# Performance work log

Measured on AMD Instinct MI355X. Metric: run time of the kernel, lower is better.

## Reference

```python
import jax, jax.numpy as jnp
import numpy as np

D = 512  # feature_dim


def setup_inputs() -> dict:
    key = jax.random.key(0)
    ks = jax.random.split(key, 16)
    B, S, P, NP = 64, 4096, 4, 4
    s = 1.0 / np.sqrt(D)
    inp = {
        "trajectory_features": jax.random.normal(ks[0], (B, S, D), dtype=jnp.float32),
        "primitive_sequence": jax.random.randint(ks[1], (P,), 0, NP),
        # primitive embedding table (num_primitives, D)
        "emb": jax.random.normal(ks[2], (NP, D), dtype=jnp.float32),
        # q/k/v projections, stored as (in, out) so y = x @ W + b
        "Wq": jax.random.uniform(ks[3], (D, D), minval=-s, maxval=s, dtype=jnp.float32),
        "bq": jax.random.uniform(ks[4], (D,), minval=-s, maxval=s, dtype=jnp.float32),
        "Wk": jax.random.uniform(ks[5], (D, D), minval=-s, maxval=s, dtype=jnp.float32),
        "bk": jax.random.uniform(ks[6], (D,), minval=-s, maxval=s, dtype=jnp.float32),
        "Wv": jax.random.uniform(ks[7], (D, D), minval=-s, maxval=s, dtype=jnp.float32),
        "bv": jax.random.uniform(ks[8], (D,), minval=-s, maxval=s, dtype=jnp.float32),
        # credit estimator MLP: Linear(2D,64) -> ReLU -> Linear(64,1) -> Sigmoid
        "W1": jax.random.uniform(ks[9], (2 * D, 64), minval=-1 / np.sqrt(2 * D), maxval=1 / np.sqrt(2 * D), dtype=jnp.float32),
        "b1": jax.random.uniform(ks[10], (64,), minval=-1 / np.sqrt(2 * D), maxval=1 / np.sqrt(2 * D), dtype=jnp.float32),
        "W2": jax.random.uniform(ks[11], (64, 1), minval=-0.125, maxval=0.125, dtype=jnp.float32),
        "b2": jax.random.uniform(ks[12], (1,), minval=-0.125, maxval=0.125, dtype=jnp.float32),
    }
    return inp


def reference(trajectory_features, primitive_sequence, emb, Wq, bq, Wk, bk, Wv, bv, W1, b1, W2, b2):
    # primitive embeddings: (P, D)
    prim = emb[primitive_sequence]
    # projections
    q = trajectory_features @ Wq + bq          # (B, S, D)
    k = prim @ Wk + bk                         # (P, D) -- shared across batch
    v = prim @ Wv + bv                         # (P, D)
    # tiny-K cross attention
    scores = jnp.einsum("bsd,pd->bsp", q, k) / jnp.sqrt(jnp.float32(D))
    attn = jax.nn.softmax(scores, axis=-1)     # (B, S, P)
    weighted = jnp.einsum("bsp,pd->bsd", attn, v)
    # concat + MLP credit head
    combined = jnp.concatenate([trajectory_features, weighted], axis=-1)  # (B, S, 2D)
    h = jax.nn.relu(combined @ W1 + b1)
    credit = jax.nn.sigmoid(h @ W2 + b2)[..., 0]  # (B, S)
    return credit, attn
```

## Files before the change

kernel.cpp:

```cpp
#include <hip/hip_runtime.h>
#include <hip/hip_bf16.h>

#define DD 512
#define OFF_K   0
#define OFF_V   8192
#define OFF_C   16384
#define OFF_VB  16448
#define OFF_KQ  17472
#define OFF_W1F 25664

typedef __attribute__((ext_vector_type(8))) __bf16 bf16x8;
typedef __attribute__((ext_vector_type(8))) float f32x8;
typedef __attribute__((ext_vector_type(4))) float f32x4;
typedef unsigned short u16;

__device__ __forceinline__ u16 f2bf(float f) {
  unsigned u = __builtin_bit_cast(unsigned, f);
  u += 0x7fffu + ((u >> 16) & 1u);
  return (u16)(u >> 16);
}

__global__ void prep_kv(const float* __restrict__ emb, const int* __restrict__ seq,
                        const float* __restrict__ Wk, const float* __restrict__ bk,
                        const float* __restrict__ Wv, const float* __restrict__ bv,
                        float* __restrict__ ws_kv) {
  __shared__ float red[8][64];
  const int b = blockIdx.x;
  const int kind = b >> 5, p = (b >> 3) & 3, dc = b & 7;
  const int dl = threadIdx.x & 63, jg = threadIdx.x >> 6;
  const int d = dc * 64 + dl;
  const float* W = kind ? Wv : Wk;
  const float* bias = kind ? bv : bk;
  const float* pr = emb + seq[p] * DD + jg * 64;
  const float* Wp = W + (size_t)(jg * 64) * DD + d;
  float a0 = 0.f, a1 = 0.f, a2 = 0.f, a3 = 0.f;
  #pragma unroll 4
  for (int j = 0; j < 64; j += 4) {
    a0 += pr[j]     * Wp[(size_t)j * DD];
    a1 += pr[j + 1] * Wp[(size_t)(j + 1) * DD];
    a2 += pr[j + 2] * Wp[(size_t)(j + 2) * DD];
    a3 += pr[j + 3] * Wp[(size_t)(j + 3) * DD];
  }
  red[jg][dl] = (a0 + a1) + (a2 + a3);
  __syncthreads();
  if (jg == 0) {
    float s = red[0][dl];
    #pragma unroll
    for (int g = 1; g < 8; ++g) s += red[g][dl];
    ws_kv[kind * 2048 + p * 512 + d] = s + bias[d];
  }
}

__global__ void prep_frag(const float* __restrict__ Wq, const float* __restrict__ bq,
                          const float* __restrict__ W1, char* __restrict__ ws) {
  const float* kk = (const float*)(ws + OFF_K);
  const float* vv = (const float*)(ws + OFF_V);
  const int b = blockIdx.x;
  const int lane = threadIdx.x & 63;
  const int wv = threadIdx.x >> 6;

  if (b < 128) {
    const int dg = b * 4 + wv;
    const f32x8 wqv = *(const f32x8*)(Wq + (size_t)dg * DD + lane * 8);
    float a[4];
    #pragma unroll
    for (int p = 0; p < 4; ++p) {
      const f32x8 kv = *(const f32x8*)(kk + p * 512 + lane * 8);
      float s = 0.f;
      #pragma unroll
      for (int j = 0; j < 8; ++j) s += wqv[j] * kv[j];
      #pragma unroll
      for (int sft = 1; sft < 64; sft <<= 1) s += __shfl_xor(s, sft, 64);
      a[p] = s;
    }
    if (lane < 4) {
      float v = lane == 0 ? a[0] : lane == 1 ? a[1] : lane == 2 ? a[2] : a[3];
      ((float*)(ws + OFF_KQ))[dg * 4 + lane] = v;
    }
  } else if (b < 192) {
    const int idx = (b - 128) * 4 + wv;
    const int p = idx >> 6, col = idx & 63;
    const f32x8 vvv = *(const f32x8*)(vv + p * 512 + lane * 8);
    float s = 0.f;
    #pragma unroll
    for (int j = 0; j < 8; ++j) s += vvv[j] * W1[(size_t)(512 + lane * 8 + j) * 64 + col];
    #pragma unroll
    for (int sft = 1; sft < 64; sft <<= 1) s += __shfl_xor(s, sft, 64);
    if (lane == 0) ((float*)(ws + OFF_VB))[p * 64 + col] = s;
  } else if (b == 192) {
    if (wv < 4) {
      const f32x8 bqv = *(const f32x8*)(bq + lane * 8);
      const f32x8 kv = *(const f32x8*)(kk + wv * 512 + lane * 8);
      float s = 0.f;
      #pragma unroll
      for (int j = 0; j < 8; ++j) s += bqv[j] * kv[j];
      #pragma unroll
      for (int sft = 1; sft < 64; sft <<= 1) s += __shfl_xor(s, sft, 64);
      if (lane == 0) ((float*)(ws + OFF_C))[wv] = s;
    }
  } else {
    const int u = (b - 193) * 256 + threadIdx.x;
    const int kt = u >> 8, ct = (u >> 6) & 3, l = u & 63;
    const int kb = kt * 32 + ((l >> 4) << 3);
    const int col = ct * 16 + (l & 15);
    u16 buf[8];
    #pragma unroll
    for (int j = 0; j < 8; ++j) buf[j] = f2bf(W1[(size_t)(kb + j) * 64 + col]);
    *(uint4*)(ws + OFF_W1F + (size_t)u * 16) = *(const uint4*)buf;
  }
}

__launch_bounds__(512, 4)
__global__ void credit_main(const float* __restrict__ x, const char* __restrict__ ws,
                            const float* __restrict__ b1, const float* __restrict__ W2,
                            const float* __restrict__ b2, float* __restrict__ out) {
  __shared__ char lds[81920];
  {
    const uint4* src = (const uint4*)(ws + OFF_W1F);
    uint4* dst = (uint4*)lds;
    #pragma unroll
    for (int i = 0; i < 8; ++i) dst[threadIdx.x + i * 512] = src[threadIdx.x + i * 512];
    const float* kq = (const float*)(ws + OFF_KQ);
    const int e0 = threadIdx.x * 16;
    const int kt = e0 >> 9;
    u16 buf[16];
    #pragma unroll
    for (int m = 0; m < 16; ++m) {
      const int e = e0 + m, l = (e >> 3) & 63, j = e & 7, p = l & 15;
      float v = 0.f;
      if (p < 4) v = kq[(kt * 32 + ((l >> 4) << 3) + j) * 4 + p];
      buf[m] = f2bf(v);
    }
    *(uint4*)(lds + 65536 + e0 * 2) = *(const uint4*)buf;
    *(uint4*)(lds + 65536 + e0 * 2 + 16) = *(const uint4*)(buf + 8);
  }
  const int l = threadIdx.x & 63;
  const int wv = threadIdx.x >> 6;
  const int q = l & 15;
  const int g = l >> 4;

  float cv = 0.f;
  if (q < 4) cv = ((const float*)(ws + OFF_C))[q];
  float vb[4][4], b1v[4], w2v[4];
  const float* vbf = (const float*)(ws + OFF_VB);
  #pragma unroll
  for (int p = 0; p < 4; ++p)
    #pragma unroll
    for (int ct = 0; ct < 4; ++ct) vb[p][ct] = vbf[p * 64 + ct * 16 + q];
  #pragma unroll
  for (int ct = 0; ct < 4; ++ct) { b1v[ct] = b1[ct * 16 + q]; w2v[ct] = W2[ct * 16 + q]; }
  const float b2v = b2[0];
  __syncthreads();

  for (int it = 0; it < 4; ++it) {
    const int rowbase = (blockIdx.x * 4 + it) * 128 + wv * 16;
    const float* xr = x + (size_t)(rowbase + q) * DD + g * 8;
    f32x4 zero = {0.f, 0.f, 0.f, 0.f};
    f32x4 acc[4];
    #pragma unroll
    for (int ct = 0; ct < 4; ++ct) acc[ct] = zero;
    f32x4 sacc = zero;

    #pragma unroll 4
    for (int kt = 0; kt < 16; ++kt) {
      const f32x8 a = *(const f32x8*)(xr + kt * 32);
      const bf16x8 af = __builtin_convertvector(a, bf16x8);
      const char* wbase = lds + (size_t)(kt * 4 * 64 + l) * 16;
      #pragma unroll
      for (int ct = 0; ct < 4; ++ct)
        acc[ct] = __builtin_amdgcn_mfma_f32_16x16x32_bf16(
            af, *(const bf16x8*)(wbase + ct * 1024), acc[ct], 0, 0, 0);
      const bf16x8 kqf = *(const bf16x8*)(lds + 65536 + (size_t)(kt * 64 + l) * 16);
      sacc = __builtin_amdgcn_mfma_f32_16x16x32_bf16(af, kqf, sacc, 0, 0, 0);
    }

    const float rs = 0.04419417382415922f;
    float attn[4];
    #pragma unroll
    for (int r = 0; r < 4; ++r) {
      float s = (sacc[r] + cv) * rs;
      float m = fmaxf(s, __shfl_xor(s, 1, 64));
      m = fmaxf(m, __shfl_xor(m, 2, 64));
      float e = __expf(s - m);
      float sm = e + __shfl_xor(e, 1, 64);
      sm += __shfl_xor(sm, 2, 64);
      attn[r] = e / sm;
    }
    if (q < 4) {
      #pragma unroll
      for (int r = 0; r < 4; ++r)
        out[262144 + (rowbase + g * 4 + r) * 4 + q] = attn[r];
    }
    float ap[4][4];
    #pragma unroll
    for (int p = 0; p < 4; ++p) {
      const int src = (l & 48) + p;
      #pragma unroll
      for (int r = 0; r < 4; ++r) ap[p][r] = __shfl(attn[r], src, 64);
    }
    float cred[4] = {0.f, 0.f, 0.f, 0.f};
    #pragma unroll
    for (int ct = 0; ct < 4; ++ct) {
      #pragma unroll
      for (int r = 0; r < 4; ++r) {
        float h = acc[ct][r] + b1v[ct];
        #pragma unroll
        for (int p = 0; p < 4; ++p) h += ap[p][r] * vb[p][ct];
        h = fmaxf(h, 0.f);
        cred[r] += h * w2v[ct];
      }
    }
    #pragma unroll
    for (int r = 0; r < 4; ++r) {
      float cz = cred[r];
      cz += __shfl_xor(cz, 1, 64);
      cz += __shfl_xor(cz, 2, 64);
      cz += __shfl_xor(cz, 4, 64);
      cz += __shfl_xor(cz, 8, 64);
      cred[r] = 1.f / (1.f + __expf(-(cz + b2v)));
    }
    if (q == 0) {
      float4 c4 = make_float4(cred[0], cred[1], cred[2], cred[3]);
      *(float4*)(out + rowbase + g * 4) = c4;
    }
  }
}

extern "C" void kernel_launch(void* const* d_in, const int* in_sizes, int n_in,
                              void* d_out, int out_size, void* d_ws, size_t ws_size,
                              hipStream_t stream) {
  const float* x   = (const float*)d_in[0];
  const int*   seq = (const int*)d_in[1];
  const float* emb = (const float*)d_in[2];
  const float* Wq  = (const float*)d_in[3];
  const float* bq  = (const float*)d_in[4];
  const float* Wk  = (const float*)d_in[5];
  const float* bk  = (const float*)d_in[6];
  const float* Wv  = (const float*)d_in[7];
  const float* bv  = (const float*)d_in[8];
  const float* W1  = (const float*)d_in[9];
  const float* b1  = (const float*)d_in[10];
  const float* W2  = (const float*)d_in[11];
  const float* b2  = (const float*)d_in[12];
  char* ws = (char*)d_ws;

  prep_kv<<<64, 512, 0, stream>>>(emb, seq, Wk, bk, Wv, bv, (float*)ws);
  prep_frag<<<209, 256, 0, stream>>>(Wq, bq, W1, ws);
  credit_main<<<512, 512, 0, stream>>>(x, ws, b1, W2, b2, (float*)d_out);
}
```

Measured before the change: 112.4 us.

## Software-pipeline x loads with nontemporal prefetch and batch primitives in prep_kv

The main kernel now holds a rotating register stage of four 8-float x loads, prefetched four k-steps ahead with nontemporal hints and carried across row iterations, so global-load latency overlaps the MFMA work. The k-loop is fully unrolled to allow this. prep_kv now computes all four primitives per weight load, which halves its block count and removes redundant reads of Wk and Wv. The costs are higher register pressure from the staging buffers, and the final iteration issues redundant prefetch loads.

```diff
diff --git a/kernel.cpp b/kernel.cpp
--- a/kernel.cpp
+++ b/kernel.cpp
@@ -19,35 +19,41 @@
   u += 0x7fffu + ((u >> 16) & 1u);
   return (u16)(u >> 16);
 }
+__device__ __forceinline__ f32x8 ntload8(const float* p) {
+  return __builtin_nontemporal_load((const f32x8*)p);
+}
 
 __global__ void prep_kv(const float* __restrict__ emb, const int* __restrict__ seq,
                         const float* __restrict__ Wk, const float* __restrict__ bk,
                         const float* __restrict__ Wv, const float* __restrict__ bv,
                         float* __restrict__ ws_kv) {
-  __shared__ float red[8][64];
+  __shared__ float red[16][32][4];
   const int b = blockIdx.x;
-  const int kind = b >> 5, p = (b >> 3) & 3, dc = b & 7;
-  const int dl = threadIdx.x & 63, jg = threadIdx.x >> 6;
-  const int d = dc * 64 + dl;
+  const int kind = b >> 4, dc = b & 15;
+  const int dl = threadIdx.x & 31, jg = threadIdx.x >> 5;
+  const int d = dc * 32 + dl;
   const float* W = kind ? Wv : Wk;
   const float* bias = kind ? bv : bk;
-  const float* pr = emb + seq[p] * DD + jg * 64;
-  const float* Wp = W + (size_t)(jg * 64) * DD + d;
+  const float* e0 = emb + seq[0] * DD + jg * 32;
+  const float* e1 = emb + seq[1] * DD + jg * 32;
+  const float* e2 = emb + seq[2] * DD + jg * 32;
+  const float* e3 = emb + seq[3] * DD + jg * 32;
+  const float* Wp = W + (size_t)(jg * 32) * DD + d;
   float a0 = 0.f, a1 = 0.f, a2 = 0.f, a3 = 0.f;
-  #pragma unroll 4
-  for (int j = 0; j < 64; j += 4) {
-    a0 += pr[j]     * Wp[(size_t)j * DD];
-    a1 += pr[j + 1] * Wp[(size_t)(j + 1) * DD];
-    a2 += pr[j + 2] * Wp[(size_t)(j + 2) * DD];
-    a3 += pr[j + 3] * Wp[(size_t)(j + 3) * DD];
-  }
-  red[jg][dl] = (a0 + a1) + (a2 + a3);
+  #pragma unroll 8
+  for (int j = 0; j < 32; ++j) {
+    const float w = Wp[(size_t)j * DD];
+    a0 += e0[j] * w; a1 += e1[j] * w; a2 += e2[j] * w; a3 += e3[j] * w;
+  }
+  f32x4 av = {a0, a1, a2, a3};
+  *(f32x4*)&red[jg][dl][0] = av;
   __syncthreads();
-  if (jg == 0) {
-    float s = red[0][dl];
-    #pragma unroll
-    for (int g = 1; g < 8; ++g) s += red[g][dl];
-    ws_kv[kind * 2048 + p * 512 + d] = s + bias[d];
+  if (threadIdx.x < 128) {
+    const int d2 = threadIdx.x & 31, p = threadIdx.x >> 5;
+    float s = 0.f;
+    #pragma unroll
+    for (int g = 0; g < 16; ++g) s += red[g][d2][p];
+    ws_kv[kind * 2048 + p * 512 + dc * 32 + d2] = s + bias[dc * 32 + d2];
   }
 }
 
@@ -152,18 +158,27 @@
   const float b2v = b2[0];
   __syncthreads();
 
+  const float* xbase = x + (size_t)(blockIdx.x * 512 + wv * 16 + q) * DD + g * 8;
+
+  f32x8 stage[4];
+  #pragma unroll
+  for (int i = 0; i < 4; ++i) stage[i] = ntload8(xbase + i * 32);
+
   for (int it = 0; it < 4; ++it) {
-    const int rowbase = (blockIdx.x * 4 + it) * 128 + wv * 16;
-    const float* xr = x + (size_t)(rowbase + q) * DD + g * 8;
+    const int rowbase = blockIdx.x * 512 + it * 128 + wv * 16;
+    const float* xr = xbase + (size_t)it * 128 * DD;
+    const float* xn = xbase + (size_t)(it < 3 ? it + 1 : it) * 128 * DD;
     f32x4 zero = {0.f, 0.f, 0.f, 0.f};
     f32x4 acc[4];
     #pragma unroll
     for (int ct = 0; ct < 4; ++ct) acc[ct] = zero;
     f32x4 sacc = zero;
 
-    #pragma unroll 4
+    #pragma unroll
     for (int kt = 0; kt < 16; ++kt) {
-      const f32x8 a = *(const f32x8*)(xr + kt * 32);
+      const f32x8 a = stage[kt & 3];
+      const float* nsrc = (kt < 12) ? (xr + (kt + 4) * 32) : (xn + (kt - 12) * 32);
+      stage[kt & 3] = ntload8(nsrc);
       const bf16x8 af = __builtin_convertvector(a, bf16x8);
       const char* wbase = lds + (size_t)(kt * 4 * 64 + l) * 16;
       #pragma unroll
@@ -244,7 +259,7 @@
   const float* b2  = (const float*)d_in[12];
   char* ws = (char*)d_ws;
 
-  prep_kv<<<64, 512, 0, stream>>>(emb, seq, Wk, bk, Wv, bv, (float*)ws);
+  prep_kv<<<32, 512, 0, stream>>>(emb, seq, Wk, bk, Wv, bv, (float*)ws);
   prep_frag<<<209, 256, 0, stream>>>(Wq, bq, W1, ws);
   credit_main<<<512, 512, 0, stream>>>(x, ws, b1, W2, b2, (float*)d_out);
 }
```

Result: slower. 353.9 us (+215.0%).
